# Performance work log

Hardware: AMD Instinct MI355X
Metric: run time of the kernel (lower is better)

Reference implementation:

```python
import jax, jax.numpy as jnp
import numpy as np

B, N, H, L, V = 512, 48, 256, 64, 800  # trees, nodes/tree (chain), hidden, latent, vocab


def _build_structure():
    # Chain tree: nodes 0..N-1; edges per tree: 2i=(i->i+1), 2i+1=(i+1->i).
    # DFS order with reverse edges: forward steps t=0..N-2 (label 0), then backtrack (label 1).
    T = 2 * (N - 1)
    Et = 2 * (N - 1)
    eid = np.zeros(T, np.int32); pred = np.zeros(T, np.int32); pm = np.zeros(T, bool)
    vl = np.zeros(T, np.int32)
    in0 = np.zeros(T, np.int32); m0 = np.zeros(T, bool)
    in1 = np.zeros(T, np.int32); m1 = np.zeros(T, bool)
    lab = np.zeros(T, np.int32)
    for t in range(N - 1):  # forward: edge (t -> t+1)
        eid[t] = 2 * t
        if t > 0:
            pred[t], pm[t] = 2 * (t - 1), True  # line-graph pred (t-1 -> t)
        v = t + 1; vl[t] = v
        in0[t], m0[t] = 2 * (v - 1), True       # in-edge (v-1 -> v)
        if v < N - 1:
            in1[t], m1[t] = 2 * v + 1, True     # in-edge (v+1 -> v), m still zero here
        lab[t] = 0
    for k in range(N - 1):  # backtrack: edge (u -> u-1)
        t = N - 1 + k; u = N - 1 - k
        eid[t] = 2 * (u - 1) + 1
        if u < N - 1:
            pred[t], pm[t] = 2 * u + 1, True    # line-graph pred (u+1 -> u)
        v = u - 1; vl[t] = v
        if v > 0:
            in0[t], m0[t] = 2 * (v - 1), True
        in1[t], m1[t] = 2 * v + 1, True
        lab[t] = 1
    eoff = (np.arange(B, dtype=np.int32) * Et)[None, :]
    noff = (np.arange(B, dtype=np.int32) * N)[None, :]
    src_l = np.empty(Et, np.int32); dst_l = np.empty(Et, np.int32)
    for i in range(N - 1):
        src_l[2 * i], dst_l[2 * i] = i, i + 1
        src_l[2 * i + 1], dst_l[2 * i + 1] = i + 1, i
    d = dict(
        step_eid=eid[:, None] + eoff,
        step_pred=pred[:, None] + eoff,
        step_pmask=np.broadcast_to(pm[:, None], (T, B)).copy(),
        step_v=vl[:, None] + noff,
        step_in0=in0[:, None] + eoff,
        step_m0=np.broadcast_to(m0[:, None], (T, B)).copy(),
        step_in1=in1[:, None] + eoff,
        step_m1=np.broadcast_to(m1[:, None], (T, B)).copy(),
        step_label=lab,
        edge_src=(src_l[None, :] + (np.arange(B, dtype=np.int32) * N)[:, None]).reshape(-1),
        edge_dst=(dst_l[None, :] + (np.arange(B, dtype=np.int32) * N)[:, None]).reshape(-1),
        root_ids=np.arange(B, dtype=np.int32) * N,
    )
    return {k: jnp.asarray(v) for k, v in d.items()}


def setup_inputs() -> dict:
    key = jax.random.key(0)
    ks = jax.random.split(key, 20)
    lin = lambda k, i, o: jax.random.normal(k, (i, o), jnp.float32) * (1.0 / np.sqrt(i))
    inp = _build_structure()
    inp['wid'] = jax.random.randint(ks[0], (B * N,), 0, V)
    inp['tree_vec'] = jax.random.normal(ks[1], (B, L), jnp.float32)
    inp['embedding'] = jax.random.normal(ks[2], (V, H), jnp.float32) * 0.1
    inp['Wz'] = lin(ks[3], 2 * H, H); inp['bz'] = jnp.zeros((H,), jnp.float32)
    inp['Wr'] = lin(ks[4], H, H)                                   # no bias (W_r)
    inp['Ur'] = lin(ks[5], H, H); inp['br'] = jnp.zeros((H,), jnp.float32)
    inp['Wh'] = lin(ks[6], 2 * H, H); inp['bh'] = jnp.zeros((H,), jnp.float32)
    inp['W_w'] = lin(ks[7], H + L, H); inp['W_b'] = jnp.zeros((H,), jnp.float32)
    inp['U_w'] = lin(ks[8], 2 * H + L, H); inp['U_b'] = jnp.zeros((H,), jnp.float32)
    inp['Wo_w'] = lin(ks[9], H, V); inp['Wo_b'] = jnp.zeros((V,), jnp.float32)
    inp['Us_w'] = lin(ks[10], H, 1); inp['Us_b'] = jnp.zeros((1,), jnp.float32)
    inp['n_fwd'] = N - 1
    return inp


def reference(wid, tree_vec, embedding, Wz, bz, Wr, Ur, br, Wh, bh,
              W_w, W_b, U_w, U_b, Wo_w, Wo_b, Us_w, Us_b,
              edge_src, edge_dst, root_ids,
              step_eid, step_pred, step_pmask, step_v,
              step_in0, step_m0, step_in1, step_m1,
              step_label, n_fwd):
    Hd = embedding.shape[1]
    Bn, Ld = tree_vec.shape
    E = edge_src.shape[0]
    x = embedding[wid]          # [n_nodes, H]
    src_x = x[edge_src]         # [E, H]
    dst_x = x[edge_dst]

    def gru_step(carry, st):
        m, rm = carry
        e = st['eid']
        pm = st['pmask'][:, None]
        s = jnp.where(pm, m[st['pred']], 0.0)        # line-graph pull of m -> s
        arm = jnp.where(pm, rm[st['pred']], 0.0)     # pull of rm -> accum_rm
        sx = src_x[e]
        z = jax.nn.sigmoid(jnp.concatenate([sx, s], 1) @ Wz + bz)
        mt = jnp.tanh(jnp.concatenate([sx, arm], 1) @ Wh + bh)
        m_e = (1.0 - z) * s + z * mt
        r = jax.nn.sigmoid(dst_x[e] @ Wr + m_e @ Ur + br)
        m = m.at[e].set(m_e)
        rm = rm.at[e].set(r * m_e)
        # node pull: h[v] = sum of m over all in-edges of v
        h_v = jnp.where(st['m0'][:, None], m[st['in0']], 0.0) \
            + jnp.where(st['m1'][:, None], m[st['in1']], 0.0)
        return (m, rm), h_v

    xs = {'eid': step_eid, 'pred': step_pred, 'pmask': step_pmask,
          'in0': step_in0, 'm0': step_m0, 'in1': step_in1, 'm1': step_m1}
    init = (jnp.zeros((E, Hd), x.dtype), jnp.zeros((E, Hd), x.dtype))
    _, hs = jax.lax.scan(gru_step, init, xs)  # [T, B, H]

    T = step_eid.shape[0]
    x_v = x[step_v]                                   # [T, B, H]
    tv = jnp.broadcast_to(tree_vec, (T, Bn, Ld))
    h_root = jnp.zeros((1, Bn, Hd), x.dtype)
    x_root = x[root_ids][None]
    p_in = jnp.concatenate([
        jnp.concatenate([x_root, h_root, tree_vec[None]], -1),
        jnp.concatenate([x_v, hs, tv], -1)], 0).reshape((T + 1) * Bn, 2 * Hd + Ld)
    p_tgt = jnp.concatenate([
        jnp.repeat((1 - step_label).astype(jnp.float32), Bn),
        jnp.zeros((Bn,), jnp.float32)])

    q_in = jnp.concatenate([
        jnp.concatenate([h_root[0], tree_vec], -1)[None],
        jnp.concatenate([hs[:n_fwd], tv[:n_fwd]], -1)], 0).reshape((n_fwd + 1) * Bn, Hd + Ld)
    q_tgt = jnp.concatenate([wid[root_ids][None], wid[step_v[:n_fwd]]], 0).reshape(-1)

    q = jax.nn.relu(q_in @ W_w + W_b) @ Wo_w + Wo_b
    p = (jax.nn.relu(p_in @ U_w + U_b) @ Us_w + Us_b)[:, 0]

    nt = jnp.float32(Bn)
    p_loss = jnp.sum(jnp.maximum(p, 0.0) - p * p_tgt + jnp.log1p(jnp.exp(-jnp.abs(p)))) / nt
    logq = jax.nn.log_softmax(q, -1)
    q_loss = -jnp.sum(jnp.take_along_axis(logq, q_tgt[:, None], 1)) / nt
    p_acc = jnp.mean(((p > 0).astype(jnp.int32) == p_tgt.astype(jnp.int32)).astype(jnp.float32))
    q_acc = jnp.mean((jnp.argmax(q, 1) == q_tgt).astype(jnp.float32))
    return q_loss, p_loss, q_acc, p_acc
```

## Files before the change

### kernel.cpp

```cpp
#include <hip/hip_runtime.h>
#include <math.h>

#define NTREE 512
#define NNODE 48
#define HD 256
#define LD 64
#define VOC 800
#define TSTEP 94
#define NFWD 47

typedef __attribute__((ext_vector_type(8))) short s8v;
typedef __attribute__((ext_vector_type(4))) float f4v;

__device__ __forceinline__ float sigm_f(float x) {
    return __builtin_amdgcn_rcpf(1.f + __expf(-x));
}
__device__ __forceinline__ float tanh_f(float x) {
    return 1.f - 2.f * __builtin_amdgcn_rcpf(1.f + __expf(2.f * x));
}

__device__ __forceinline__ float bfu(unsigned short u) {
    union { unsigned int i; float f; } c; c.i = ((unsigned int)u) << 16; return c.f;
}
__device__ __forceinline__ unsigned short f2bf(float f) {
    union { float f; unsigned int u; } c; c.f = f;
    return (unsigned short)((c.u + 0x7fffu + ((c.u >> 16) & 1u)) >> 16);
}
__device__ __forceinline__ s8v frag(const unsigned short* p) {
    union { int4 i; s8v v; } u; u.i = *(const int4*)p; return u.v;
}
__device__ __forceinline__ s8v zfrag() {
    union { int4 i; s8v v; } u; u.i = make_int4(0, 0, 0, 0); return u.v;
}
__device__ __forceinline__ void bar_lgkm() {
    asm volatile("s_waitcnt lgkmcnt(0)\n\ts_barrier" ::: "memory");
}

#define PV 8
__global__ __launch_bounds__(256) void prep_xproj(
    const float* __restrict__ emb,
    const float* __restrict__ Wz, const float* __restrict__ bz,
    const float* __restrict__ Wh, const float* __restrict__ bh,
    const float* __restrict__ Wr, const float* __restrict__ br,
    float* __restrict__ xzT, float* __restrict__ xhT, float* __restrict__ xrT)
{
    __shared__ float embL[PV][HD];
    const int j = threadIdx.x;
    const int v0 = blockIdx.x * PV;
    for (int r = 0; r < PV; ++r) embL[r][j] = emb[(v0 + r) * HD + j];
    __syncthreads();

    float az[PV], ah[PV], ar[PV];
#pragma unroll
    for (int r = 0; r < PV; ++r) { az[r] = bz[j]; ah[r] = bh[j]; ar[r] = br[j]; }
    for (int i = 0; i < HD; i += 4) {
        float wz0 = Wz[(i + 0) * HD + j], wz1 = Wz[(i + 1) * HD + j];
        float wz2 = Wz[(i + 2) * HD + j], wz3 = Wz[(i + 3) * HD + j];
        float wh0 = Wh[(i + 0) * HD + j], wh1 = Wh[(i + 1) * HD + j];
        float wh2 = Wh[(i + 2) * HD + j], wh3 = Wh[(i + 3) * HD + j];
        float wr0 = Wr[(i + 0) * HD + j], wr1 = Wr[(i + 1) * HD + j];
        float wr2 = Wr[(i + 2) * HD + j], wr3 = Wr[(i + 3) * HD + j];
#pragma unroll
        for (int r = 0; r < PV; ++r) {
            float4 e = *(const float4*)&embL[r][i];
            az[r] += e.x * wz0 + e.y * wz1 + e.z * wz2 + e.w * wz3;
            ah[r] += e.x * wh0 + e.y * wh1 + e.z * wh2 + e.w * wh3;
            ar[r] += e.x * wr0 + e.y * wr1 + e.z * wr2 + e.w * wr3;
        }
    }
#pragma unroll
    for (int r = 0; r < PV; ++r) {
        xzT[(v0 + r) * HD + j] = az[r];
        xhT[(v0 + r) * HD + j] = ah[r];
        xrT[(v0 + r) * HD + j] = ar[r];
    }
}

__global__ __launch_bounds__(256) void prep_misc(
    const float* __restrict__ Wz, const float* __restrict__ Wh,
    const float* __restrict__ Ur,
    const float* __restrict__ Ww, const float* __restrict__ Wow,
    const float* __restrict__ Uw,
    const float* __restrict__ emb, const float* __restrict__ tv,
    unsigned short* __restrict__ WzT, unsigned short* __restrict__ WhT,
    unsigned short* __restrict__ UrT,
    unsigned short* __restrict__ W1T, unsigned short* __restrict__ WoT,
    unsigned short* __restrict__ UwT,
    unsigned short* __restrict__ embB, unsigned short* __restrict__ tvB,
    float* __restrict__ acc)
{
    int b = blockIdx.x;
    if (b < 4) {
        acc[b * 256 + threadIdx.x] = 0.f;
    } else if (b < 772) {
        int bb = b - 4;
        const int which = bb >> 8, n = bb & 255, k = threadIdx.x;
        const float* src = (which == 0) ? (Wz + HD * HD) : (which == 1) ? (Wh + HD * HD) : Ur;
        unsigned short* dst = (which == 0) ? WzT : (which == 1) ? WhT : UrT;
        dst[n * HD + k] = f2bf(src[k * HD + n]);
    } else if (b < 2084) {
        int bb = b - 772;
        if (bb < 256) {
            for (int k = threadIdx.x; k < 320; k += 256)
                W1T[bb * 320 + k] = f2bf(Ww[k * 256 + bb]);
        } else if (bb < 1056) {
            int n = bb - 256;
            WoT[n * 256 + threadIdx.x] = f2bf(Wow[threadIdx.x * VOC + n]);
        } else {
            int n = bb - 1056;
            for (int k = threadIdx.x; k < 576; k += 256)
                UwT[n * 576 + k] = f2bf(Uw[k * 256 + n]);
        }
    } else {
        int idx = (b - 2084) * 256 + threadIdx.x;
        if (idx < VOC * HD) embB[idx] = f2bf(emb[idx]);
        else {
            int i2 = idx - VOC * HD;
            if (i2 < NTREE * LD) tvB[i2] = f2bf(tv[i2]);
        }
    }
}

__global__ __launch_bounds__(512, 2) void gru10(
    const int* __restrict__ wid,
    const float* __restrict__ xzT, const float* __restrict__ xhT,
    const float* __restrict__ xrT,
    const unsigned short* __restrict__ WzT, const unsigned short* __restrict__ WhT,
    const unsigned short* __restrict__ UrT,
    unsigned short* __restrict__ hsb)
{
    __shared__ unsigned short urL[16 * 8 * 64 * 8];
    __shared__ unsigned short mBL[2][2][HD], armBL[2][2][HD];
    __shared__ int widL[2][NNODE];

    const int tid = threadIdx.x;
    const int wave = tid >> 6, lane = tid & 63;
    const int lq = lane >> 4, ln = lane & 15;
    const int b0 = blockIdx.x * 2;
    const int T0 = 2 * wave, T1 = T0 + 1;
    const int ftree = lane >> 5;
    const int fcol  = wave * 32 + (lane & 31);
    const int srcl  = lane & 15;
    const bool hi16 = (lane & 16) != 0;
    const bool hi32 = (lane & 32) != 0;

    if (tid < 2 * NNODE) widL[tid / NNODE][tid % NNODE] =
        wid[(b0 + tid / NNODE) * NNODE + (tid % NNODE)];

#pragma unroll
    for (int s = 0; s < 16; ++s) {
        *(int4*)&urL[((s * 8 + wave) * 64 + lane) * 8] =
            *(const int4*)&UrT[(s * 16 + ln) * HD + wave * 32 + lq * 8];
    }

    s8v wz0[8], wz1[8], wh0[8], wh1[8];
#pragma unroll
    for (int kt = 0; kt < 8; ++kt) {
        const int ko = kt * 32 + lq * 8;
        wz0[kt] = frag(&WzT[(T0 * 16 + ln) * HD + ko]);
        wz1[kt] = frag(&WzT[(T1 * 16 + ln) * HD + ko]);
        wh0[kt] = frag(&WhT[(T0 * 16 + ln) * HD + ko]);
        wh1[kt] = frag(&WhT[(T1 * 16 + ln) * HD + ko]);
    }
    __syncthreads();

    float cxz, cxh, cxr, chsp = 0.f, me = 0.f;
    float nxz = 0.f, nxh = 0.f, nxr = 0.f, nhsp = 0.f;
    {
        const int ws = widL[ftree][0], wd = widL[ftree][1];
        cxz = xzT[ws * HD + fcol];
        cxh = xhT[ws * HD + fcol];
        cxr = xrT[wd * HD + fcol];
    }

#pragma unroll 2
    for (int t = 0; t < TSTEP; ++t) {
        const int par = t & 1, nxt = par ^ 1;
        const bool fwd = t < NFWD;
        const bool hp = (t != 0) && (t != NFWD);

        {
            if (t == NFWD)
                chsp = bfu(hsb[((NFWD - 2) * NTREE + b0 + ftree) * HD + fcol]);
            const int tn = t + 1;
            if (tn < TSTEP) {
                const bool fwdn = tn < NFWD;
                const int un = TSTEP - tn;
                const int srcn = fwdn ? tn : un;
                const int dstn = fwdn ? (tn + 1) : (un - 1);
                const int ws = widL[ftree][srcn], wd = widL[ftree][dstn];
                nxz = xzT[ws * HD + fcol];
                nxh = xhT[ws * HD + fcol];
                nxr = xrT[wd * HD + fcol];
                nhsp = 0.f;
                if (tn > NFWD && dstn > 0)
                    nhsp = bfu(hsb[((dstn - 1) * NTREE + b0 + ftree) * HD + fcol]);
            }
        }

        float az = 0.f, ah = 0.f;
        if (hp) {
            f4v cz0 = (f4v){0.f,0.f,0.f,0.f}, cz1 = cz0, ch0 = cz0, ch1 = cz0;
#pragma unroll
            for (int kt = 0; kt < 8; ++kt) {
                const int ko = kt * 32 + lq * 8;
                s8v am = (ln < 2) ? frag(&mBL[par][ln][ko]) : zfrag();
                s8v aa = (ln < 2) ? frag(&armBL[par][ln][ko]) : zfrag();
                cz0 = __builtin_amdgcn_mfma_f32_16x16x32_bf16(am, wz0[kt], cz0, 0, 0, 0);
                cz1 = __builtin_amdgcn_mfma_f32_16x16x32_bf16(am, wz1[kt], cz1, 0, 0, 0);
                ch0 = __builtin_amdgcn_mfma_f32_16x16x32_bf16(aa, wh0[kt], ch0, 0, 0, 0);
                ch1 = __builtin_amdgcn_mfma_f32_16x16x32_bf16(aa, wh1[kt], ch1, 0, 0, 0);
            }
            float a00 = __shfl(cz0[0], srcl), a01 = __shfl(cz0[1], srcl);
            float a10 = __shfl(cz1[0], srcl), a11 = __shfl(cz1[1], srcl);
            az = hi16 ? (hi32 ? a11 : a10) : (hi32 ? a01 : a00);
            float h00 = __shfl(ch0[0], srcl), h01 = __shfl(ch0[1], srcl);
            float h10 = __shfl(ch1[0], srcl), h11 = __shfl(ch1[1], srcl);
            ah = hi16 ? (hi32 ? h11 : h10) : (hi32 ? h01 : h00);
        }

        {
            float azv = cxz, ahv = cxh, sold = 0.f;
            if (hp) { azv += az; ahv += ah; sold = me; }
            float z = sigm_f(azv), mt = tanh_f(ahv);
            me = sold + z * (mt - sold);
            float hv = fwd ? me : (me + chsp);
            hsb[(t * NTREE + b0 + ftree) * HD + fcol] = f2bf(hv);
            mBL[nxt][ftree][fcol] = f2bf(me);
        }
        bar_lgkm();

        {
            f4v cr0 = (f4v){0.f,0.f,0.f,0.f}, cr1 = cr0;
#pragma unroll
            for (int kt = 0; kt < 8; ++kt) {
                const int ko = kt * 32 + lq * 8;
                s8v a = (ln < 2) ? frag(&mBL[nxt][ln][ko]) : zfrag();
                s8v b0f = frag(&urL[((T0 * 8 + kt) * 64 + lane) * 8]);
                s8v b1f = frag(&urL[((T1 * 8 + kt) * 64 + lane) * 8]);
                cr0 = __builtin_amdgcn_mfma_f32_16x16x32_bf16(a, b0f, cr0, 0, 0, 0);
                cr1 = __builtin_amdgcn_mfma_f32_16x16x32_bf16(a, b1f, cr1, 0, 0, 0);
            }
            float r00 = __shfl(cr0[0], srcl), r01 = __shfl(cr0[1], srcl);
            float r10 = __shfl(cr1[0], srcl), r11 = __shfl(cr1[1], srcl);
            float ar = hi16 ? (hi32 ? r11 : r10) : (hi32 ? r01 : r00);
            float r = sigm_f(cxr + ar);
            armBL[nxt][ftree][fcol] = f2bf(r * me);
            cxz = nxz; cxh = nxh; cxr = nxr; chsp = nhsp;
        }
        bar_lgkm();
    }
}

#define QG 32
#define PG 32
struct QSmem {
    unsigned short X1L[QG][328];
    unsigned short hidL[QG][264];
    int tgts[QG];
    float wred[4][QG][4];
};
struct PSmem {
    unsigned short XL[PG][584];
    int widL[PG];
    float wredp[4][PG];
};

__global__ __launch_bounds__(256) void heads(
    const int* __restrict__ wid,
    const unsigned short* __restrict__ tvB,
    const unsigned short* __restrict__ embB,
    const unsigned short* __restrict__ hsb,
    const unsigned short* __restrict__ W1T,
    const unsigned short* __restrict__ WoT,
    const unsigned short* __restrict__ UwT,
    const float* __restrict__ Wb, const float* __restrict__ Wob,
    const float* __restrict__ Ub,
    const float* __restrict__ Usw, const float* __restrict__ Usb,
    float* __restrict__ acc)
{
    __shared__ __align__(16) char smem[sizeof(QSmem) > sizeof(PSmem) ? sizeof(QSmem) : sizeof(PSmem)];
    const int tid = threadIdx.x;
    const int wave = tid >> 6, lane = tid & 63;
    const int lq = lane >> 4, ln = lane & 15;

    if (blockIdx.x < 768) {
        QSmem& S = *(QSmem*)smem;
        const int trow = blockIdx.x >> 4;
        const int b0 = (blockIdx.x & 15) * QG;

        if (tid < QG) S.tgts[tid] = wid[(b0 + tid) * NNODE + trow];
        if (trow == 0) {
            int4 z = make_int4(0, 0, 0, 0);
            for (int idx = tid; idx < QG * 32; idx += 256) {
                int m = idx >> 5, c = idx & 31;
                *(int4*)&S.X1L[m][c * 8] = z;
            }
        } else {
            const unsigned short* hrow = hsb + (size_t)(trow - 1) * NTREE * HD;
            for (int idx = tid; idx < QG * 32; idx += 256) {
                int m = idx >> 5, c = idx & 31;
                *(int4*)&S.X1L[m][c * 8] = *(const int4*)&hrow[(b0 + m) * HD + c * 8];
            }
        }
        for (int idx = tid; idx < QG * 8; idx += 256) {
            int m = idx >> 3, c = idx & 7;
            *(int4*)&S.X1L[m][256 + c * 8] = *(const int4*)&tvB[(b0 + m) * LD + c * 8];
        }
        __syncthreads();

        f4v acc1[2][4];
#pragma unroll
        for (int mt = 0; mt < 2; ++mt)
#pragma unroll
            for (int nt = 0; nt < 4; ++nt) acc1[mt][nt] = (f4v){0.f, 0.f, 0.f, 0.f};
#pragma unroll
        for (int kt = 0; kt < 10; ++kt) {
            s8v a0 = frag(&S.X1L[ln][kt * 32 + lq * 8]);
            s8v a1 = frag(&S.X1L[16 + ln][kt * 32 + lq * 8]);
#pragma unroll
            for (int nt = 0; nt < 4; ++nt) {
                int n = wave * 64 + nt * 16 + ln;
                s8v b = frag(&W1T[n * 320 + kt * 32 + lq * 8]);
                acc1[0][nt] = __builtin_amdgcn_mfma_f32_16x16x32_bf16(a0, b, acc1[0][nt], 0, 0, 0);
                acc1[1][nt] = __builtin_amdgcn_mfma_f32_16x16x32_bf16(a1, b, acc1[1][nt], 0, 0, 0);
            }
        }
#pragma unroll
        for (int nt = 0; nt < 4; ++nt) {
            int col = wave * 64 + nt * 16 + ln;
            float wb = Wb[col];
#pragma unroll
            for (int mt = 0; mt < 2; ++mt)
#pragma unroll
                for (int r = 0; r < 4; ++r)
                    S.hidL[mt * 16 + lq * 4 + r][col] = f2bf(fmaxf(acc1[mt][nt][r] + wb, 0.f));
        }
        __syncthreads();

        s8v ha0[8], ha1[8];
#pragma unroll
        for (int kt = 0; kt < 8; ++kt) {
            ha0[kt] = frag(&S.hidL[ln][kt * 32 + lq * 8]);
            ha1[kt] = frag(&S.hidL[16 + ln][kt * 32 + lq * 8]);
        }

        int rt[2][4];
#pragma unroll
        for (int mt = 0; mt < 2; ++mt)
#pragma unroll
            for (int r = 0; r < 4; ++r) rt[mt][r] = S.tgts[mt * 16 + lq * 4 + r];
        float mx[2][4], ls[2][4], tg[2][4]; int am[2][4];
#pragma unroll
        for (int mt = 0; mt < 2; ++mt)
#pragma unroll
            for (int r = 0; r < 4; ++r) { mx[mt][r] = -1e30f; ls[mt][r] = 0.f; tg[mt][r] = 0.f; am[mt][r] = 1 << 30; }

        for (int nt = wave; nt < 50; nt += 4) {
            int n = nt * 16 + ln;
            const unsigned short* wrow = WoT + n * 256;
            f4v a2[2];
            a2[0] = (f4v){0.f, 0.f, 0.f, 0.f}; a2[1] = (f4v){0.f, 0.f, 0.f, 0.f};
#pragma unroll
            for (int kt = 0; kt < 8; ++kt) {
                s8v b = frag(&wrow[kt * 32 + lq * 8]);
                a2[0] = __builtin_amdgcn_mfma_f32_16x16x32_bf16(ha0[kt], b, a2[0], 0, 0, 0);
                a2[1] = __builtin_amdgcn_mfma_f32_16x16x32_bf16(ha1[kt], b, a2[1], 0, 0, 0);
            }
            float bias = Wob[n];
#pragma unroll
            for (int mt = 0; mt < 2; ++mt)
#pragma unroll
                for (int r = 0; r < 4; ++r) {
                    float v = a2[mt][r] + bias;
                    if (n == rt[mt][r]) tg[mt][r] = v;
                    float d = v - mx[mt][r];
                    float e = __expf(-fabsf(d));
                    bool newmax = d > 0.f;
                    ls[mt][r] = fmaf(ls[mt][r], newmax ? e : 1.f, newmax ? 1.f : e);
                    if (newmax) { mx[mt][r] = v; am[mt][r] = n; }
                }
        }

#pragma unroll
        for (int s = 1; s < 16; s <<= 1) {
#pragma unroll
            for (int mt = 0; mt < 2; ++mt)
#pragma unroll
                for (int r = 0; r < 4; ++r) {
                    float mo = __shfl_xor(mx[mt][r], s);
                    float lo = __shfl_xor(ls[mt][r], s);
                    int   ao = __shfl_xor(am[mt][r], s);
                    float to = __shfl_xor(tg[mt][r], s);
                    tg[mt][r] += to;
                    float nm = fmaxf(mx[mt][r], mo);
                    ls[mt][r] = ls[mt][r] * __expf(mx[mt][r] - nm) + lo * __expf(mo - nm);
                    if (mo > mx[mt][r] || (mo == mx[mt][r] && ao < am[mt][r])) am[mt][r] = ao;
                    mx[mt][r] = nm;
                }
        }
        if (ln == 0) {
#pragma unroll
            for (int mt = 0; mt < 2; ++mt)
#pragma unroll
                for (int r = 0; r < 4; ++r) {
                    int row = mt * 16 + lq * 4 + r;
                    S.wred[wave][row][0] = mx[mt][r];
                    S.wred[wave][row][1] = ls[mt][r];
                    S.wred[wave][row][2] = __int_as_float(am[mt][r]);
                    S.wred[wave][row][3] = tg[mt][r];
                }
        }
        __syncthreads();

        float lossv = 0.f, corrv = 0.f;
        if (tid < QG) {
            float m_ = -1e30f, l_ = 0.f, t_ = 0.f; int a_ = 1 << 30;
#pragma unroll
            for (int w = 0; w < 4; ++w) {
                float mo = S.wred[w][tid][0], lo = S.wred[w][tid][1], to = S.wred[w][tid][3];
                int ao = __float_as_int(S.wred[w][tid][2]);
                t_ += to;
                float nm = fmaxf(m_, mo);
                l_ = l_ * __expf(m_ - nm) + lo * __expf(mo - nm);
                if (mo > m_ || (mo == m_ && ao < a_)) a_ = ao;
                m_ = nm;
            }
            lossv = m_ + logf(l_) - t_;
            corrv = (a_ == S.tgts[tid]) ? 1.f : 0.f;
        }
        if (wave == 0) {
            for (int s = 32; s; s >>= 1) {
                lossv += __shfl_down(lossv, s);
                corrv += __shfl_down(corrv, s);
            }
            if (tid == 0) {
                int slot = blockIdx.x & 255;
                atomicAdd(&acc[0 * 256 + slot], lossv);
                atomicAdd(&acc[2 * 256 + slot], corrv);
            }
        }
    } else {
        PSmem& S = *(PSmem*)smem;
        const int pb = blockIdx.x - 768;
        const int trow = pb >> 4;
        const int b0 = (pb & 15) * PG;
        const int node = (trow == 0) ? 0 : ((trow <= NFWD) ? trow : (TSTEP - trow));

        if (tid < PG) S.widL[tid] = wid[(b0 + tid) * NNODE + node];
        __syncthreads();

        for (int idx = tid; idx < PG * 32; idx += 256) {
            int m = idx >> 5, c = idx & 31;
            *(int4*)&S.XL[m][c * 8] = *(const int4*)&embB[S.widL[m] * HD + c * 8];
        }
        if (trow == 0) {
            int4 z = make_int4(0, 0, 0, 0);
            for (int idx = tid; idx < PG * 32; idx += 256) {
                int m = idx >> 5, c = idx & 31;
                *(int4*)&S.XL[m][256 + c * 8] = z;
            }
        } else {
            const unsigned short* hrow = hsb + (size_t)(trow - 1) * NTREE * HD;
            for (int idx = tid; idx < PG * 32; idx += 256) {
                int m = idx >> 5, c = idx & 31;
                *(int4*)&S.XL[m][256 + c * 8] = *(const int4*)&hrow[(b0 + m) * HD + c * 8];
            }
        }
        for (int idx = tid; idx < PG * 8; idx += 256) {
            int m = idx >> 3, c = idx & 7;
            *(int4*)&S.XL[m][512 + c * 8] = *(const int4*)&tvB[(b0 + m) * LD + c * 8];
        }
        __syncthreads();

        f4v a1[2][4];
#pragma unroll
        for (int mt = 0; mt < 2; ++mt)
#pragma unroll
            for (int nt = 0; nt < 4; ++nt) a1[mt][nt] = (f4v){0.f, 0.f, 0.f, 0.f};
        for (int kt = 0; kt < 18; ++kt) {
            s8v a0 = frag(&S.XL[ln][kt * 32 + lq * 8]);
            s8v am_ = frag(&S.XL[16 + ln][kt * 32 + lq * 8]);
#pragma unroll
            for (int nt = 0; nt < 4; ++nt) {
                int n = wave * 64 + nt * 16 + ln;
                s8v b = frag(&UwT[n * 576 + kt * 32 + lq * 8]);
                a1[0][nt] = __builtin_amdgcn_mfma_f32_16x16x32_bf16(a0, b, a1[0][nt], 0, 0, 0);
                a1[1][nt] = __builtin_amdgcn_mfma_f32_16x16x32_bf16(am_, b, a1[1][nt], 0, 0, 0);
            }
        }
        float part[2][4] = {{0, 0, 0, 0}, {0, 0, 0, 0}};
#pragma unroll
        for (int nt = 0; nt < 4; ++nt) {
            int n = wave * 64 + nt * 16 + ln;
            float ub = Ub[n], us = Usw[n];
#pragma unroll
            for (int mt = 0; mt < 2; ++mt)
#pragma unroll
                for (int r = 0; r < 4; ++r)
                    part[mt][r] += fmaxf(a1[mt][nt][r] + ub, 0.f) * us;
        }
#pragma unroll
        for (int s = 1; s < 16; s <<= 1) {
#pragma unroll
            for (int mt = 0; mt < 2; ++mt)
#pragma unroll
                for (int r = 0; r < 4; ++r)
                    part[mt][r] += __shfl_xor(part[mt][r], s);
        }
        if (ln == 0) {
#pragma unroll
            for (int mt = 0; mt < 2; ++mt)
#pragma unroll
                for (int r = 0; r < 4; ++r)
                    S.wredp[wave][mt * 16 + lq * 4 + r] = part[mt][r];
        }
        __syncthreads();

        float lossv = 0.f, corrv = 0.f;
        if (tid < PG) {
            float p = S.wredp[0][tid] + S.wredp[1][tid] + S.wredp[2][tid] + S.wredp[3][tid] + Usb[0];
            float tgt = (trow < NFWD) ? 1.f : 0.f;
            lossv = fmaxf(p, 0.f) - p * tgt + log1pf(expf(-fabsf(p)));
            corrv = (((p > 0.f) ? 1 : 0) == ((trow < NFWD) ? 1 : 0)) ? 1.f : 0.f;
        }
        if (wave == 0) {
            for (int s = 32; s; s >>= 1) {
                lossv += __shfl_down(lossv, s);
                corrv += __shfl_down(corrv, s);
            }
            if (tid == 0) {
                int slot = blockIdx.x & 255;
                atomicAdd(&acc[1 * 256 + slot], lossv);
                atomicAdd(&acc[3 * 256 + slot], corrv);
            }
        }
    }
}

__global__ void fin_kernel(const float* __restrict__ acc, float* __restrict__ out) {
    const int tid = threadIdx.x;
    const int c = tid >> 6, lane = tid & 63;
    float v = 0.f;
    for (int i = lane; i < 256; i += 64) v += acc[c * 256 + i];
    for (int s = 32; s; s >>= 1) v += __shfl_down(v, s);
    if (lane == 0) {
        const float sc[4] = {1.f / 512.f, 1.f / 512.f, 1.f / 24576.f, 1.f / 48640.f};
        out[c] = v * sc[c];
    }
}

extern "C" void kernel_launch(void* const* d_in, const int* in_sizes, int n_in,
                              void* d_out, int out_size, void* d_ws, size_t ws_size,
                              hipStream_t stream) {
    const int*   wid  = (const int*)  d_in[12];
    const float* tv   = (const float*)d_in[13];
    const float* emb  = (const float*)d_in[14];
    const float* Wz   = (const float*)d_in[15];
    const float* bz   = (const float*)d_in[16];
    const float* Wr   = (const float*)d_in[17];
    const float* Ur   = (const float*)d_in[18];
    const float* br   = (const float*)d_in[19];
    const float* Wh   = (const float*)d_in[20];
    const float* bh   = (const float*)d_in[21];
    const float* Ww   = (const float*)d_in[22];
    const float* Wb   = (const float*)d_in[23];
    const float* Uw   = (const float*)d_in[24];
    const float* Ubias= (const float*)d_in[25];
    const float* Wow  = (const float*)d_in[26];
    const float* Wob  = (const float*)d_in[27];
    const float* Usw  = (const float*)d_in[28];
    const float* Usb  = (const float*)d_in[29];

    char* w = (char*)d_ws;
    float* accb = (float*)w;
    float* xzT  = (float*)(w + 4096);
    float* xhT  = (float*)(w + 823296);
    float* xrT  = (float*)(w + 1642496);
    unsigned short* WzT2 = (unsigned short*)(w + 2461696);
    unsigned short* WhT2 = (unsigned short*)(w + 2592768);
    unsigned short* UrT2 = (unsigned short*)(w + 2723840);
    unsigned short* hsb  = (unsigned short*)(w + 2854912);
    unsigned short* W1T  = (unsigned short*)(w + 27496448);
    unsigned short* WoT  = (unsigned short*)(w + 27660288);
    unsigned short* UwT  = (unsigned short*)(w + 28069888);
    unsigned short* embB = (unsigned short*)(w + 28364800);
    unsigned short* tvB  = (unsigned short*)(w + 28774400);

    prep_xproj<<<VOC / PV, 256, 0, stream>>>(emb, Wz, bz, Wh, bh, Wr, br, xzT, xhT, xrT);
    prep_misc<<<3012, 256, 0, stream>>>(Wz, Wh, Ur, Ww, Wow, Uw, emb, tv,
                                        WzT2, WhT2, UrT2, W1T, WoT, UwT,
                                        embB, tvB, accb);
    gru10<<<NTREE / 2, 512, 0, stream>>>(wid, xzT, xhT, xrT, WzT2, WhT2, UrT2, hsb);
    heads<<<768 + 1520, 256, 0, stream>>>(wid, tvB, embB, hsb, W1T, WoT, UwT,
                                          Wb, Wob, Ubias, Usw, Usb, accb);
    fin_kernel<<<1, 256, 0, stream>>>(accb, (float*)d_out);
}
```

Measured before the change: 448.1 us.

## Merge xproj prep into prep_misc and double-buffer weight fragments in heads

Folds the embedding-projection prep kernel into the misc prep kernel as extra blocks, removing one launch and letting the two prep jobs run concurrently. In the heads kernel, the global weight fragments for the W, Wo and Uw MFMA loops are now prefetched one iteration ahead into double-buffered registers, so load latency overlaps with MFMA work. The cost is higher register pressure, which could lower occupancy, and prep_misc now reserves shared memory for every block.

```diff
diff --git a/kernel.cpp b/kernel.cpp
--- a/kernel.cpp
+++ b/kernel.cpp
@@ -37,47 +37,10 @@
 }
 
 #define PV 8
-__global__ __launch_bounds__(256) void prep_xproj(
-    const float* __restrict__ emb,
+__global__ __launch_bounds__(256) void prep_misc(
     const float* __restrict__ Wz, const float* __restrict__ bz,
     const float* __restrict__ Wh, const float* __restrict__ bh,
     const float* __restrict__ Wr, const float* __restrict__ br,
-    float* __restrict__ xzT, float* __restrict__ xhT, float* __restrict__ xrT)
-{
-    __shared__ float embL[PV][HD];
-    const int j = threadIdx.x;
-    const int v0 = blockIdx.x * PV;
-    for (int r = 0; r < PV; ++r) embL[r][j] = emb[(v0 + r) * HD + j];
-    __syncthreads();
-
-    float az[PV], ah[PV], ar[PV];
-#pragma unroll
-    for (int r = 0; r < PV; ++r) { az[r] = bz[j]; ah[r] = bh[j]; ar[r] = br[j]; }
-    for (int i = 0; i < HD; i += 4) {
-        float wz0 = Wz[(i + 0) * HD + j], wz1 = Wz[(i + 1) * HD + j];
-        float wz2 = Wz[(i + 2) * HD + j], wz3 = Wz[(i + 3) * HD + j];
-        float wh0 = Wh[(i + 0) * HD + j], wh1 = Wh[(i + 1) * HD + j];
-        float wh2 = Wh[(i + 2) * HD + j], wh3 = Wh[(i + 3) * HD + j];
-        float wr0 = Wr[(i + 0) * HD + j], wr1 = Wr[(i + 1) * HD + j];
-        float wr2 = Wr[(i + 2) * HD + j], wr3 = Wr[(i + 3) * HD + j];
-#pragma unroll
-        for (int r = 0; r < PV; ++r) {
-            float4 e = *(const float4*)&embL[r][i];
-            az[r] += e.x * wz0 + e.y * wz1 + e.z * wz2 + e.w * wz3;
-            ah[r] += e.x * wh0 + e.y * wh1 + e.z * wh2 + e.w * wh3;
-            ar[r] += e.x * wr0 + e.y * wr1 + e.z * wr2 + e.w * wr3;
-        }
-    }
-#pragma unroll
-    for (int r = 0; r < PV; ++r) {
-        xzT[(v0 + r) * HD + j] = az[r];
-        xhT[(v0 + r) * HD + j] = ah[r];
-        xrT[(v0 + r) * HD + j] = ar[r];
-    }
-}
-
-__global__ __launch_bounds__(256) void prep_misc(
-    const float* __restrict__ Wz, const float* __restrict__ Wh,
     const float* __restrict__ Ur,
     const float* __restrict__ Ww, const float* __restrict__ Wow,
     const float* __restrict__ Uw,
@@ -87,8 +50,10 @@
     unsigned short* __restrict__ W1T, unsigned short* __restrict__ WoT,
     unsigned short* __restrict__ UwT,
     unsigned short* __restrict__ embB, unsigned short* __restrict__ tvB,
+    float* __restrict__ xzT, float* __restrict__ xhT, float* __restrict__ xrT,
     float* __restrict__ acc)
 {
+    __shared__ float embL[PV][HD];
     int b = blockIdx.x;
     if (b < 4) {
         acc[b * 256 + threadIdx.x] = 0.f;
@@ -111,12 +76,42 @@
             for (int k = threadIdx.x; k < 576; k += 256)
                 UwT[n * 576 + k] = f2bf(Uw[k * 256 + n]);
         }
-    } else {
+    } else if (b < 3012) {
         int idx = (b - 2084) * 256 + threadIdx.x;
         if (idx < VOC * HD) embB[idx] = f2bf(emb[idx]);
         else {
             int i2 = idx - VOC * HD;
             if (i2 < NTREE * LD) tvB[i2] = f2bf(tv[i2]);
+        }
+    } else {
+        const int j = threadIdx.x;
+        const int v0 = (b - 3012) * PV;
+        for (int r = 0; r < PV; ++r) embL[r][j] = emb[(v0 + r) * HD + j];
+        __syncthreads();
+
+        float az[PV], ah[PV], ar[PV];
+#pragma unroll
+        for (int r = 0; r < PV; ++r) { az[r] = bz[j]; ah[r] = bh[j]; ar[r] = br[j]; }
+        for (int i = 0; i < HD; i += 4) {
+            float wz0 = Wz[(i + 0) * HD + j], wz1 = Wz[(i + 1) * HD + j];
+            float wz2 = Wz[(i + 2) * HD + j], wz3 = Wz[(i + 3) * HD + j];
+            float wh0 = Wh[(i + 0) * HD + j], wh1 = Wh[(i + 1) * HD + j];
+            float wh2 = Wh[(i + 2) * HD + j], wh3 = Wh[(i + 3) * HD + j];
+            float wr0 = Wr[(i + 0) * HD + j], wr1 = Wr[(i + 1) * HD + j];
+            float wr2 = Wr[(i + 2) * HD + j], wr3 = Wr[(i + 3) * HD + j];
+#pragma unroll
+            for (int r = 0; r < PV; ++r) {
+                float4 e = *(const float4*)&embL[r][i];
+                az[r] += e.x * wz0 + e.y * wz1 + e.z * wz2 + e.w * wz3;
+                ah[r] += e.x * wh0 + e.y * wh1 + e.z * wh2 + e.w * wh3;
+                ar[r] += e.x * wr0 + e.y * wr1 + e.z * wr2 + e.w * wr3;
+            }
+        }
+#pragma unroll
+        for (int r = 0; r < PV; ++r) {
+            xzT[(v0 + r) * HD + j] = az[r];
+            xhT[(v0 + r) * HD + j] = ah[r];
+            xrT[(v0 + r) * HD + j] = ar[r];
         }
     }
 }
@@ -314,16 +309,24 @@
         for (int mt = 0; mt < 2; ++mt)
 #pragma unroll
             for (int nt = 0; nt < 4; ++nt) acc1[mt][nt] = (f4v){0.f, 0.f, 0.f, 0.f};
+        s8v bq[2][4];
+#pragma unroll
+        for (int nt = 0; nt < 4; ++nt)
+            bq[0][nt] = frag(&W1T[(wave * 64 + nt * 16 + ln) * 320 + lq * 8]);
 #pragma unroll
         for (int kt = 0; kt < 10; ++kt) {
+            const int cur = kt & 1, nx = cur ^ 1;
+            if (kt < 9) {
+#pragma unroll
+                for (int nt = 0; nt < 4; ++nt)
+                    bq[nx][nt] = frag(&W1T[(wave * 64 + nt * 16 + ln) * 320 + (kt + 1) * 32 + lq * 8]);
+            }
             s8v a0 = frag(&S.X1L[ln][kt * 32 + lq * 8]);
             s8v a1 = frag(&S.X1L[16 + ln][kt * 32 + lq * 8]);
 #pragma unroll
             for (int nt = 0; nt < 4; ++nt) {
-                int n = wave * 64 + nt * 16 + ln;
-                s8v b = frag(&W1T[n * 320 + kt * 32 + lq * 8]);
-                acc1[0][nt] = __builtin_amdgcn_mfma_f32_16x16x32_bf16(a0, b, acc1[0][nt], 0, 0, 0);
-                acc1[1][nt] = __builtin_amdgcn_mfma_f32_16x16x32_bf16(a1, b, acc1[1][nt], 0, 0, 0);
+                acc1[0][nt] = __builtin_amdgcn_mfma_f32_16x16x32_bf16(a0, bq[cur][nt], acc1[0][nt], 0, 0, 0);
+                acc1[1][nt] = __builtin_amdgcn_mfma_f32_16x16x32_bf16(a1, bq[cur][nt], acc1[1][nt], 0, 0, 0);
             }
         }
 #pragma unroll
@@ -356,16 +359,27 @@
 #pragma unroll
             for (int r = 0; r < 4; ++r) { mx[mt][r] = -1e30f; ls[mt][r] = 0.f; tg[mt][r] = 0.f; am[mt][r] = 1 << 30; }
 
+        s8v bo[2][8];
+        {
+            const unsigned short* w0 = WoT + (wave * 16 + ln) * 256;
+#pragma unroll
+            for (int kt = 0; kt < 8; ++kt) bo[0][kt] = frag(&w0[kt * 32 + lq * 8]);
+        }
+        int pb = 0;
         for (int nt = wave; nt < 50; nt += 4) {
+            const int cur = pb, nx = pb ^ 1; pb ^= 1;
+            if (nt + 4 < 50) {
+                const unsigned short* wn = WoT + ((nt + 4) * 16 + ln) * 256;
+#pragma unroll
+                for (int kt = 0; kt < 8; ++kt) bo[nx][kt] = frag(&wn[kt * 32 + lq * 8]);
+            }
             int n = nt * 16 + ln;
-            const unsigned short* wrow = WoT + n * 256;
             f4v a2[2];
             a2[0] = (f4v){0.f, 0.f, 0.f, 0.f}; a2[1] = (f4v){0.f, 0.f, 0.f, 0.f};
 #pragma unroll
             for (int kt = 0; kt < 8; ++kt) {
-                s8v b = frag(&wrow[kt * 32 + lq * 8]);
-                a2[0] = __builtin_amdgcn_mfma_f32_16x16x32_bf16(ha0[kt], b, a2[0], 0, 0, 0);
-                a2[1] = __builtin_amdgcn_mfma_f32_16x16x32_bf16(ha1[kt], b, a2[1], 0, 0, 0);
+                a2[0] = __builtin_amdgcn_mfma_f32_16x16x32_bf16(ha0[kt], bo[cur][kt], a2[0], 0, 0, 0);
+                a2[1] = __builtin_amdgcn_mfma_f32_16x16x32_bf16(ha1[kt], bo[cur][kt], a2[1], 0, 0, 0);
             }
             float bias = Wob[n];
 #pragma unroll
@@ -442,9 +456,9 @@
         }
     } else {
         PSmem& S = *(PSmem*)smem;
-        const int pb = blockIdx.x - 768;
-        const int trow = pb >> 4;
-        const int b0 = (pb & 15) * PG;
+        const int pb_ = blockIdx.x - 768;
+        const int trow = pb_ >> 4;
+        const int b0 = (pb_ & 15) * PG;
         const int node = (trow == 0) ? 0 : ((trow <= NFWD) ? trow : (TSTEP - trow));
 
         if (tid < PG) S.widL[tid] = wid[(b0 + tid) * NNODE + node];
@@ -478,15 +492,23 @@
         for (int mt = 0; mt < 2; ++mt)
 #pragma unroll
             for (int nt = 0; nt < 4; ++nt) a1[mt][nt] = (f4v){0.f, 0.f, 0.f, 0.f};
+        s8v bp[2][4];
+#pragma unroll
+        for (int nt = 0; nt < 4; ++nt)
+            bp[0][nt] = frag(&UwT[(wave * 64 + nt * 16 + ln) * 576 + lq * 8]);
         for (int kt = 0; kt < 18; ++kt) {
+            const int cur = kt & 1, nx = cur ^ 1;
+            if (kt < 17) {
+#pragma unroll
+                for (int nt = 0; nt < 4; ++nt)
+                    bp[nx][nt] = frag(&UwT[(wave * 64 + nt * 16 + ln) * 576 + (kt + 1) * 32 + lq * 8]);
+            }
             s8v a0 = frag(&S.XL[ln][kt * 32 + lq * 8]);
             s8v am_ = frag(&S.XL[16 + ln][kt * 32 + lq * 8]);
 #pragma unroll
             for (int nt = 0; nt < 4; ++nt) {
-                int n = wave * 64 + nt * 16 + ln;
-                s8v b = frag(&UwT[n * 576 + kt * 32 + lq * 8]);
-                a1[0][nt] = __builtin_amdgcn_mfma_f32_16x16x32_bf16(a0, b, a1[0][nt], 0, 0, 0);
-                a1[1][nt] = __builtin_amdgcn_mfma_f32_16x16x32_bf16(am_, b, a1[1][nt], 0, 0, 0);
+                a1[0][nt] = __builtin_amdgcn_mfma_f32_16x16x32_bf16(a0, bp[cur][nt], a1[0][nt], 0, 0, 0);
+                a1[1][nt] = __builtin_amdgcn_mfma_f32_16x16x32_bf16(am_, bp[cur][nt], a1[1][nt], 0, 0, 0);
             }
         }
         float part[2][4] = {{0, 0, 0, 0}, {0, 0, 0, 0}};
@@ -587,10 +609,9 @@
     unsigned short* embB = (unsigned short*)(w + 28364800);
     unsigned short* tvB  = (unsigned short*)(w + 28774400);
 
-    prep_xproj<<<VOC / PV, 256, 0, stream>>>(emb, Wz, bz, Wh, bh, Wr, br, xzT, xhT, xrT);
-    prep_misc<<<3012, 256, 0, stream>>>(Wz, Wh, Ur, Ww, Wow, Uw, emb, tv,
-                                        WzT2, WhT2, UrT2, W1T, WoT, UwT,
-                                        embB, tvB, accb);
+    prep_misc<<<3112, 256, 0, stream>>>(Wz, bz, Wh, bh, Wr, br, Ur, Ww, Wow, Uw,
+                                        emb, tv, WzT2, WhT2, UrT2, W1T, WoT, UwT,
+                                        embB, tvB, xzT, xhT, xrT, accb);
     gru10<<<NTREE / 2, 512, 0, stream>>>(wid, xzT, xhT, xrT, WzT2, WhT2, UrT2, hsb);
     heads<<<768 + 1520, 256, 0, stream>>>(wid, tvB, embB, hsb, W1T, WoT, UwT,
                                           Wb, Wob, Ubias, Usw, Usb, accb);
```

Result: slower. 508.6 us (+13.5%).

## Run forward and backtrack GRU chains concurrently, add fixup for residual sum

Applied to the files above, without the earlier changes.

On a chain tree the backtrack messages do not depend on the forward messages, so the backtrack step's recurrence is independent. The change runs both chains together in one loop of 47 steps, packing 4 rows (2 trees × 2 directions) into the MFMA A operand instead of 2. This halves the number of serial steps. The residual add of the forward hidden state to backtrack outputs moves into a separate elementwise fixup kernel, which adds one extra launch and some memory traffic.

```diff
diff --git a/kernel.cpp b/kernel.cpp
--- a/kernel.cpp
+++ b/kernel.cpp
@@ -121,7 +121,8 @@
     }
 }
 
-__global__ __launch_bounds__(512, 2) void gru10(
+#define ASTR 264
+__global__ __launch_bounds__(512, 2) void gru12(
     const int* __restrict__ wid,
     const float* __restrict__ xzT, const float* __restrict__ xhT,
     const float* __restrict__ xrT,
@@ -130,7 +131,7 @@
     unsigned short* __restrict__ hsb)
 {
     __shared__ unsigned short urL[16 * 8 * 64 * 8];
-    __shared__ unsigned short mBL[2][2][HD], armBL[2][2][HD];
+    __shared__ unsigned short mBL[2][4][ASTR], armBL[2][4][ASTR];
     __shared__ int widL[2][NNODE];
 
     const int tid = threadIdx.x;
@@ -164,69 +165,73 @@
     }
     __syncthreads();
 
-    float cxz, cxh, cxr, chsp = 0.f, me = 0.f;
-    float nxz = 0.f, nxh = 0.f, nxr = 0.f, nhsp = 0.f;
+    float cxz[2], cxh[2], cxr[2], me2[2] = {0.f, 0.f};
+    float nxz[2] = {0.f, 0.f}, nxh[2] = {0.f, 0.f}, nxr[2] = {0.f, 0.f};
     {
-        const int ws = widL[ftree][0], wd = widL[ftree][1];
-        cxz = xzT[ws * HD + fcol];
-        cxh = xhT[ws * HD + fcol];
-        cxr = xrT[wd * HD + fcol];
-    }
-
-#pragma unroll 2
-    for (int t = 0; t < TSTEP; ++t) {
-        const int par = t & 1, nxt = par ^ 1;
-        const bool fwd = t < NFWD;
-        const bool hp = (t != 0) && (t != NFWD);
+        cxz[0] = xzT[widL[ftree][0] * HD + fcol];
+        cxh[0] = xhT[widL[ftree][0] * HD + fcol];
+        cxr[0] = xrT[widL[ftree][1] * HD + fcol];
+        cxz[1] = xzT[widL[ftree][47] * HD + fcol];
+        cxh[1] = xhT[widL[ftree][47] * HD + fcol];
+        cxr[1] = xrT[widL[ftree][46] * HD + fcol];
+    }
+
+    for (int s = 0; s < NFWD; ++s) {
+        const int par = s & 1, nxt = par ^ 1;
+        const bool hp = (s != 0);
 
         {
-            if (t == NFWD)
-                chsp = bfu(hsb[((NFWD - 2) * NTREE + b0 + ftree) * HD + fcol]);
-            const int tn = t + 1;
-            if (tn < TSTEP) {
-                const bool fwdn = tn < NFWD;
-                const int un = TSTEP - tn;
-                const int srcn = fwdn ? tn : un;
-                const int dstn = fwdn ? (tn + 1) : (un - 1);
-                const int ws = widL[ftree][srcn], wd = widL[ftree][dstn];
-                nxz = xzT[ws * HD + fcol];
-                nxh = xhT[ws * HD + fcol];
-                nxr = xrT[wd * HD + fcol];
-                nhsp = 0.f;
-                if (tn > NFWD && dstn > 0)
-                    nhsp = bfu(hsb[((dstn - 1) * NTREE + b0 + ftree) * HD + fcol]);
-            }
-        }
-
-        float az = 0.f, ah = 0.f;
+            const int sn = s + 1;
+            if (sn < NFWD) {
+                const int un = NFWD - sn;
+                nxz[0] = xzT[widL[ftree][sn] * HD + fcol];
+                nxh[0] = xhT[widL[ftree][sn] * HD + fcol];
+                nxr[0] = xrT[widL[ftree][sn + 1] * HD + fcol];
+                nxz[1] = xzT[widL[ftree][un] * HD + fcol];
+                nxh[1] = xhT[widL[ftree][un] * HD + fcol];
+                nxr[1] = xrT[widL[ftree][un - 1] * HD + fcol];
+            }
+        }
+
+        float az[2] = {0.f, 0.f}, ah[2] = {0.f, 0.f};
         if (hp) {
             f4v cz0 = (f4v){0.f,0.f,0.f,0.f}, cz1 = cz0, ch0 = cz0, ch1 = cz0;
 #pragma unroll
             for (int kt = 0; kt < 8; ++kt) {
                 const int ko = kt * 32 + lq * 8;
-                s8v am = (ln < 2) ? frag(&mBL[par][ln][ko]) : zfrag();
-                s8v aa = (ln < 2) ? frag(&armBL[par][ln][ko]) : zfrag();
+                s8v am = (ln < 4) ? frag(&mBL[par][ln][ko]) : zfrag();
+                s8v aa = (ln < 4) ? frag(&armBL[par][ln][ko]) : zfrag();
                 cz0 = __builtin_amdgcn_mfma_f32_16x16x32_bf16(am, wz0[kt], cz0, 0, 0, 0);
                 cz1 = __builtin_amdgcn_mfma_f32_16x16x32_bf16(am, wz1[kt], cz1, 0, 0, 0);
                 ch0 = __builtin_amdgcn_mfma_f32_16x16x32_bf16(aa, wh0[kt], ch0, 0, 0, 0);
                 ch1 = __builtin_amdgcn_mfma_f32_16x16x32_bf16(aa, wh1[kt], ch1, 0, 0, 0);
             }
-            float a00 = __shfl(cz0[0], srcl), a01 = __shfl(cz0[1], srcl);
-            float a10 = __shfl(cz1[0], srcl), a11 = __shfl(cz1[1], srcl);
-            az = hi16 ? (hi32 ? a11 : a10) : (hi32 ? a01 : a00);
-            float h00 = __shfl(ch0[0], srcl), h01 = __shfl(ch0[1], srcl);
-            float h10 = __shfl(ch1[0], srcl), h11 = __shfl(ch1[1], srcl);
-            ah = hi16 ? (hi32 ? h11 : h10) : (hi32 ? h01 : h00);
+            float f0 = __shfl(cz0[0], srcl), f1 = __shfl(cz0[1], srcl);
+            float g0 = __shfl(cz1[0], srcl), g1 = __shfl(cz1[1], srcl);
+            az[0] = hi16 ? (hi32 ? g1 : g0) : (hi32 ? f1 : f0);
+            float f2 = __shfl(cz0[2], srcl), f3 = __shfl(cz0[3], srcl);
+            float g2 = __shfl(cz1[2], srcl), g3 = __shfl(cz1[3], srcl);
+            az[1] = hi16 ? (hi32 ? g3 : g2) : (hi32 ? f3 : f2);
+            float h0 = __shfl(ch0[0], srcl), h1 = __shfl(ch0[1], srcl);
+            float i0 = __shfl(ch1[0], srcl), i1 = __shfl(ch1[1], srcl);
+            ah[0] = hi16 ? (hi32 ? i1 : i0) : (hi32 ? h1 : h0);
+            float h2 = __shfl(ch0[2], srcl), h3 = __shfl(ch0[3], srcl);
+            float i2 = __shfl(ch1[2], srcl), i3 = __shfl(ch1[3], srcl);
+            ah[1] = hi16 ? (hi32 ? i3 : i2) : (hi32 ? h3 : h2);
         }
 
         {
-            float azv = cxz, ahv = cxh, sold = 0.f;
-            if (hp) { azv += az; ahv += ah; sold = me; }
-            float z = sigm_f(azv), mt = tanh_f(ahv);
-            me = sold + z * (mt - sold);
-            float hv = fwd ? me : (me + chsp);
-            hsb[(t * NTREE + b0 + ftree) * HD + fcol] = f2bf(hv);
-            mBL[nxt][ftree][fcol] = f2bf(me);
+#pragma unroll
+            for (int c = 0; c < 2; ++c) {
+                float azv = cxz[c], ahv = cxh[c], sold = 0.f;
+                if (hp) { azv += az[c]; ahv += ah[c]; sold = me2[c]; }
+                float z = sigm_f(azv), mt = tanh_f(ahv);
+                float me = sold + z * (mt - sold);
+                const int row = (c == 0) ? s : (NFWD + s);
+                hsb[((size_t)row * NTREE + b0 + ftree) * HD + fcol] = f2bf(me);
+                mBL[nxt][c * 2 + ftree][fcol] = f2bf(me);
+                me2[c] = me;
+            }
         }
         bar_lgkm();
 
@@ -235,21 +240,43 @@
 #pragma unroll
             for (int kt = 0; kt < 8; ++kt) {
                 const int ko = kt * 32 + lq * 8;
-                s8v a = (ln < 2) ? frag(&mBL[nxt][ln][ko]) : zfrag();
+                s8v a = (ln < 4) ? frag(&mBL[nxt][ln][ko]) : zfrag();
                 s8v b0f = frag(&urL[((T0 * 8 + kt) * 64 + lane) * 8]);
                 s8v b1f = frag(&urL[((T1 * 8 + kt) * 64 + lane) * 8]);
                 cr0 = __builtin_amdgcn_mfma_f32_16x16x32_bf16(a, b0f, cr0, 0, 0, 0);
                 cr1 = __builtin_amdgcn_mfma_f32_16x16x32_bf16(a, b1f, cr1, 0, 0, 0);
             }
-            float r00 = __shfl(cr0[0], srcl), r01 = __shfl(cr0[1], srcl);
-            float r10 = __shfl(cr1[0], srcl), r11 = __shfl(cr1[1], srcl);
-            float ar = hi16 ? (hi32 ? r11 : r10) : (hi32 ? r01 : r00);
-            float r = sigm_f(cxr + ar);
-            armBL[nxt][ftree][fcol] = f2bf(r * me);
-            cxz = nxz; cxh = nxh; cxr = nxr; chsp = nhsp;
+            float f0 = __shfl(cr0[0], srcl), f1 = __shfl(cr0[1], srcl);
+            float g0 = __shfl(cr1[0], srcl), g1 = __shfl(cr1[1], srcl);
+            float ar0 = hi16 ? (hi32 ? g1 : g0) : (hi32 ? f1 : f0);
+            float f2 = __shfl(cr0[2], srcl), f3 = __shfl(cr0[3], srcl);
+            float g2 = __shfl(cr1[2], srcl), g3 = __shfl(cr1[3], srcl);
+            float ar1 = hi16 ? (hi32 ? g3 : g2) : (hi32 ? f3 : f2);
+            armBL[nxt][0 * 2 + ftree][fcol] = f2bf(sigm_f(cxr[0] + ar0) * me2[0]);
+            armBL[nxt][1 * 2 + ftree][fcol] = f2bf(sigm_f(cxr[1] + ar1) * me2[1]);
+#pragma unroll
+            for (int c = 0; c < 2; ++c) {
+                cxz[c] = nxz[c]; cxh[c] = nxh[c]; cxr[c] = nxr[c];
+            }
         }
         bar_lgkm();
     }
+}
+
+__global__ __launch_bounds__(256) void fixup(unsigned short* __restrict__ hsb)
+{
+    const int k = blockIdx.x >> 7;
+    const int chunk = blockIdx.x & 127;
+    const size_t off = (size_t)chunk * 1024 + threadIdx.x * 4;
+    const size_t tgt = (size_t)(NFWD + k) * NTREE * HD + off;
+    const size_t src = (size_t)(NFWD - 2 - k) * NTREE * HD + off;
+    ushort4 a = *(ushort4*)&hsb[tgt];
+    ushort4 c = *(const ushort4*)&hsb[src];
+    a.x = f2bf(bfu(a.x) + bfu(c.x));
+    a.y = f2bf(bfu(a.y) + bfu(c.y));
+    a.z = f2bf(bfu(a.z) + bfu(c.z));
+    a.w = f2bf(bfu(a.w) + bfu(c.w));
+    *(ushort4*)&hsb[tgt] = a;
 }
 
 #define QG 32
@@ -591,7 +618,8 @@
     prep_misc<<<3012, 256, 0, stream>>>(Wz, Wh, Ur, Ww, Wow, Uw, emb, tv,
                                         WzT2, WhT2, UrT2, W1T, WoT, UwT,
                                         embB, tvB, accb);
-    gru10<<<NTREE / 2, 512, 0, stream>>>(wid, xzT, xhT, xrT, WzT2, WhT2, UrT2, hsb);
+    gru12<<<NTREE / 2, 512, 0, stream>>>(wid, xzT, xhT, xrT, WzT2, WhT2, UrT2, hsb);
+    fixup<<<46 * 128, 256, 0, stream>>>(hsb);
     heads<<<768 + 1520, 256, 0, stream>>>(wid, tvB, embB, hsb, W1T, WoT, UwT,
                                           Wb, Wob, Ubias, Usw, Usb, accb);
     fin_kernel<<<1, 256, 0, stream>>>(accb, (float*)d_out);
```

New measurement: 383.5 us. -14.4%, faster.
